# Kernel optimization log

Measured on AMD Instinct MI355X. Metric: run time of the kernel, lower is better.

## Reference

```python
import jax, jax.numpy as jnp
import numpy as np
import math

B, S, D, H = 4, 2048, 1024, 16
HD = D // H  # head_dim = 64


def setup_inputs() -> dict:
    key = jax.random.key(0)
    ks = jax.random.split(key, 12)
    inv = 1.0 / math.sqrt(D)
    inp = {
        "query": jax.random.normal(ks[0], (B, S, D), dtype=jnp.float32),
        "key": jax.random.normal(ks[1], (B, S, D), dtype=jnp.float32),
        "value": jax.random.normal(ks[2], (B, S, D), dtype=jnp.float32),
        # causal mask, broadcast over heads; guarantees no all-masked softmax rows
        "mask": jnp.tril(jnp.ones((S, S), dtype=jnp.int32))[None, None].repeat(B, axis=0),
        # linear params stored as (in, out); y = x @ W + b (same math as torch Linear)
        "Wq": jax.random.uniform(ks[3], (D, D), jnp.float32, -inv, inv),
        "bq": jax.random.uniform(ks[4], (D,), jnp.float32, -inv, inv),
        "Wk": jax.random.uniform(ks[5], (D, D), jnp.float32, -inv, inv),
        "bk": jax.random.uniform(ks[6], (D,), jnp.float32, -inv, inv),
        "Wv": jax.random.uniform(ks[7], (D, D), jnp.float32, -inv, inv),
        "bv": jax.random.uniform(ks[8], (D,), jnp.float32, -inv, inv),
        "Wo": jax.random.uniform(ks[9], (D, D), jnp.float32, -inv, inv),
        "bo": jax.random.uniform(ks[10], (D,), jnp.float32, -inv, inv),
    }
    return inp


def _split_heads(x):
    # [B, S, D] -> [B, H, S, HD]
    b, s, _ = x.shape
    return x.reshape(b, s, H, HD).transpose(0, 2, 1, 3)


def reference(query, key, value, mask, Wq, bq, Wk, bk, Wv, bv, Wo, bo):
    q = _split_heads(query @ Wq + bq)   # [B,H,S,HD]
    k = _split_heads(key @ Wk + bk)
    v = _split_heads(value @ Wv + bv)
    scores = jnp.einsum("bhqd,bhkd->bhqk", q, k)          # [B,H,S,S]
    scores = jnp.where(mask == 0, -jnp.inf, scores)
    attn = jax.nn.softmax(scores / math.sqrt(HD), axis=-1)
    attn = attn * mask.astype(attn.dtype)                  # post-softmax re-mask (as in source)
    out = jnp.einsum("bhqk,bhkd->bhqd", attn, v)           # [B,H,S,HD]
    out = out.transpose(0, 2, 1, 3).reshape(query.shape[0], -1, D)
    return out @ Wo + bo
```

## Files before the change

kernel.cpp:

```cpp
#include <hip/hip_runtime.h>

typedef __attribute__((ext_vector_type(8))) short short8;
typedef __attribute__((ext_vector_type(8))) unsigned short ushort8;
typedef __attribute__((ext_vector_type(4))) unsigned short us4;
typedef __attribute__((ext_vector_type(4))) float f32x4;
typedef __attribute__((ext_vector_type(4))) int i32x4;

#define S_LEN 2048
#define D_MODEL 1024
#define N_HEADS 16
#define HEAD_DIM 64

__device__ __forceinline__ unsigned short f2bf(float f) {
  union { float f; unsigned u; } x; x.f = f;
  unsigned r = x.u + 0x7FFFu + ((x.u >> 16) & 1u);
  return (unsigned short)(r >> 16);
}

__device__ __forceinline__ int pkbf(float a, float b) {
  union { float f; unsigned u; } x, y;
  x.f = a; y.f = b;
  return (int)__builtin_amdgcn_perm(y.u + 0x8000u, x.u + 0x8000u, 0x07060302u);
}

__global__ __launch_bounds__(256) void cvt3_kernel(const float* __restrict__ a,
                                                   const float* __restrict__ b,
                                                   const float* __restrict__ c,
                                                   unsigned short* __restrict__ oa,
                                                   unsigned short* __restrict__ ob,
                                                   unsigned short* __restrict__ oc) {
  int bid = blockIdx.x;
  const float* in = (bid < 4096) ? a : (bid < 8192 ? b : c);
  unsigned short* out = (bid < 4096) ? oa : (bid < 8192 ? ob : oc);
  int i = (bid & 4095) * 256 + threadIdx.x;
  const f32x4* in4 = (const f32x4*)in;
  f32x4 x = in4[2 * i], y = in4[2 * i + 1];
  i32x4 o;
  o[0] = pkbf(x[0], x[1]);
  o[1] = pkbf(x[2], x[3]);
  o[2] = pkbf(y[0], y[1]);
  o[3] = pkbf(y[2], y[3]);
  ((i32x4*)out)[i] = o;
}

__global__ __launch_bounds__(256) void transpose_w4(
    const float* __restrict__ Wq, const float* __restrict__ Wk,
    const float* __restrict__ Wv, const float* __restrict__ Wo,
    unsigned short* __restrict__ wqkvT, unsigned short* __restrict__ woT) {
  __shared__ float tile[64][65];
  const int z = blockIdx.z;
  const float* W = (z == 0) ? Wq : (z == 1) ? Wk : (z == 2) ? Wv : Wo;
  unsigned short* Wt = (z < 3) ? (wqkvT + (size_t)z * D_MODEL * D_MODEL) : woT;
  const int no = blockIdx.x * 64, ko = blockIdx.y * 64;
  const int tx = threadIdx.x & 63, ty = threadIdx.x >> 6;
  for (int r = ty; r < 64; r += 4)
    tile[r][tx] = W[(size_t)(ko + r) * D_MODEL + no + tx];
  __syncthreads();
  for (int r = ty; r < 64; r += 4)
    Wt[(size_t)(no + r) * D_MODEL + ko + tx] = f2bf(tile[tx][r]);
}

template <int MODE>
__global__ __launch_bounds__(256, (MODE == 0 ? 2 : 3)) void proj_gemm(
    const unsigned short* __restrict__ A0,
    const unsigned short* __restrict__ A1,
    const unsigned short* __restrict__ A2,
    const unsigned short* __restrict__ Bt,
    const float* __restrict__ b0p, const float* __restrict__ b1p,
    const float* __restrict__ b2p,
    void* __restrict__ o0, void* __restrict__ o1, void* __restrict__ o2,
    float qscale) {
  constexpr int NJ = (MODE == 0) ? 8 : 4;
  constexpr int BN = NJ * 32;
  constexpr int BUFS = 4096 + NJ * 1024;
  constexpr int NBI = NJ / 2;
  extern __shared__ __align__(16) unsigned short smem_d[];
  const int tid = threadIdx.x;
  const int wave = tid >> 6, lane = tid & 63;
  const int quad = lane >> 4, l16 = lane & 15;

  const int GX = (MODE == 0) ? 12 : 8;
  const int nlin = blockIdx.y * GX + blockIdx.x;
  const int xcd = nlin & 7;
  const int j = nlin >> 3;
  int bx_eff, by_eff;
  if (MODE == 0) { by_eff = xcd * 8 + j / 12; bx_eff = j % 12; }
  else           { by_eff = xcd * 8 + (j >> 3); bx_eff = j & 7; }
  const int m0 = by_eff * 128, n0 = bx_eff * BN;
  const int wm = (wave >> 1) * 64, wn = (wave & 1) * (NJ * 16);

  const int sel = (MODE == 0) ? (n0 >> 10) : 0;
  const unsigned short* A = (MODE == 0) ? (sel == 0 ? A0 : sel == 1 ? A1 : A2) : A0;
  const float* bias = (MODE == 0) ? (sel == 0 ? b0p : sel == 1 ? b1p : b2p) : b0p;
  const float scale = (MODE == 0 && sel == 0) ? qscale : 1.0f;
  const int nb = (MODE == 0) ? (n0 & 1023) : n0;

  f32x4 acc[4][NJ] = {};

  const int lrow = lane >> 2;
  const int kcs = ((lane & 3) ^ ((lane >> 3) & 3)) << 3;

  auto stage = [&](int kt, int bsel) {
    unsigned short* Ab = smem_d + bsel * BUFS;
    unsigned short* Bb = Ab + 4096;
    const int k0 = kt * 32;
#pragma unroll
    for (int c = 0; c < 2; ++c) {
      const int r = wave * 32 + c * 16;
      const unsigned short* ga = A + (size_t)(m0 + r + lrow) * D_MODEL + k0 + kcs;
      __builtin_amdgcn_global_load_lds((const __attribute__((address_space(1))) void*)ga,
          (__attribute__((address_space(3))) void*)(Ab + r * 32), 16, 0, 0);
    }
#pragma unroll
    for (int c = 0; c < NBI; ++c) {
      const int r = wave * (BN / 4) + c * 16;
      const unsigned short* gb = Bt + (size_t)(n0 + r + lrow) * D_MODEL + k0 + kcs;
      __builtin_amdgcn_global_load_lds((const __attribute__((address_space(1))) void*)gb,
          (__attribute__((address_space(3))) void*)(Bb + r * 32), 16, 0, 0);
    }
  };

  const int fsw = (quad ^ ((l16 >> 1) & 3)) << 3;

  stage(0, 0); stage(1, 1); stage(2, 2);
  if constexpr (MODE == 0) { asm volatile("s_waitcnt vmcnt(12)" ::: "memory"); }
  else                     { asm volatile("s_waitcnt vmcnt(8)" ::: "memory"); }
  __builtin_amdgcn_s_barrier();
  __builtin_amdgcn_sched_barrier(0);

  for (int kt = 0; kt < 32; ++kt) {
    const int bsel = kt % 3;
    const unsigned short* Ab = smem_d + bsel * BUFS;
    const unsigned short* Bb = Ab + 4096;
    short8 af[4], bf[NJ];
#pragma unroll
    for (int i = 0; i < 4; ++i)
      af[i] = *(const short8*)(Ab + (wm + i * 16 + l16) * 32 + fsw);
#pragma unroll
    for (int j2 = 0; j2 < NJ; ++j2)
      bf[j2] = *(const short8*)(Bb + (wn + j2 * 16 + l16) * 32 + fsw);
    asm volatile("s_waitcnt lgkmcnt(0)" ::: "memory");
    __builtin_amdgcn_s_barrier();
    __builtin_amdgcn_sched_barrier(0);
    if (kt + 3 < 32) stage(kt + 3, bsel);
    __builtin_amdgcn_s_setprio(1);
#pragma unroll
    for (int i = 0; i < 4; ++i)
#pragma unroll
      for (int j2 = 0; j2 < NJ; ++j2)
        acc[i][j2] = __builtin_amdgcn_mfma_f32_16x16x32_bf16(af[i], bf[j2], acc[i][j2], 0, 0, 0);
    __builtin_amdgcn_s_setprio(0);
    if constexpr (MODE == 0) {
      if (kt + 3 < 32)      { asm volatile("s_waitcnt vmcnt(12)" ::: "memory"); }
      else if (kt + 2 < 32) { asm volatile("s_waitcnt vmcnt(6)" ::: "memory"); }
      else if (kt + 1 < 32) { asm volatile("s_waitcnt vmcnt(0)" ::: "memory"); }
    } else {
      if (kt + 3 < 32)      { asm volatile("s_waitcnt vmcnt(8)" ::: "memory"); }
      else if (kt + 2 < 32) { asm volatile("s_waitcnt vmcnt(4)" ::: "memory"); }
      else if (kt + 1 < 32) { asm volatile("s_waitcnt vmcnt(0)" ::: "memory"); }
    }
    __builtin_amdgcn_s_barrier();
    __builtin_amdgcn_sched_barrier(0);
  }

  float bv[NJ];
#pragma unroll
  for (int j2 = 0; j2 < NJ; ++j2) bv[j2] = bias[nb + wn + j2 * 16 + l16];

  if constexpr (MODE == 0) {
    if (sel < 2) {
      unsigned short* T = smem_d + wave * 2176;
      unsigned short* out = (unsigned short*)(sel == 0 ? o0 : o1);
      const int h0 = (nb + wn) >> 6;
#pragma unroll
      for (int i = 0; i < 4; ++i) {
#pragma unroll
        for (int j2 = 0; j2 < 8; ++j2)
#pragma unroll
          for (int r = 0; r < 4; ++r)
            T[(quad * 4 + r) * 136 + j2 * 16 + l16] = f2bf((acc[i][j2][r] + bv[j2]) * scale);
        int m = m0 + wm + i * 16 + l16;
        int b = m >> 11, s = m & 2047;
#pragma unroll
        for (int t = 0; t < 4; ++t) {
          short8 row = *(const short8*)(T + l16 * 136 + t * 32 + quad * 8);
          int c = t * 32 + quad * 8;
          int h = h0 + (c >> 6), d = c & 63;
          *(short8*)(out + (((size_t)(b * N_HEADS + h) * S_LEN + s) << 6) + d) = row;
        }
      }
    } else {
      unsigned short* vt = (unsigned short*)o2;
#pragma unroll
      for (int i = 0; i < 4; ++i) {
        int m = m0 + wm + i * 16 + quad * 4;
        int b = m >> 11, s = m & 2047;
#pragma unroll
        for (int j2 = 0; j2 < 8; ++j2) {
          int n = nb + wn + j2 * 16 + l16;
          int h = n >> 6, d = n & 63;
          us4 pv;
#pragma unroll
          for (int r = 0; r < 4; ++r) pv[r] = f2bf(acc[i][j2][r] + bv[j2]);
          *(us4*)(vt + (((size_t)(b * N_HEADS + h) * 64 + d) << 11) + s) = pv;
        }
      }
    }
  } else {
    float* Tf = (float*)smem_d + wave * 1088;
    float* out = (float*)o0;
#pragma unroll
    for (int i = 0; i < 4; ++i) {
#pragma unroll
      for (int j2 = 0; j2 < 4; ++j2)
#pragma unroll
        for (int r = 0; r < 4; ++r)
          Tf[(quad * 4 + r) * 68 + j2 * 16 + l16] = acc[i][j2][r] + bv[j2];
      int m = m0 + wm + i * 16 + l16;
#pragma unroll
      for (int t = 0; t < 4; ++t) {
        f32x4 row = *(const f32x4*)(Tf + l16 * 68 + t * 16 + quad * 4);
        *(f32x4*)(out + (size_t)m * D_MODEL + nb + wn + t * 16 + quad * 4) = row;
      }
    }
  }
}

__global__ __launch_bounds__(256, 4) void flash_attn(
    const unsigned short* __restrict__ Qh,
    const unsigned short* __restrict__ Kh,
    const unsigned short* __restrict__ Vt,
    unsigned short* __restrict__ ctx) {
  __shared__ __align__(16) unsigned short smem[16384];
  const int tid = threadIdx.x;
  const int wave = tid >> 6, lane = tid & 63;
  const int quad = lane >> 4, l16 = lane & 15;
  const int l7 = l16 & 7;

  const int nlin = blockIdx.y * 16 + blockIdx.x;
  const int xcd = nlin & 7;
  const int rr = nlin >> 3;
  const int bh = xcd * 8 + (rr & 7);
  const int qslot = rr >> 3;
  const int qa = qslot & 3, qb = qslot >> 2;
  const int qbase = qa + ((qb >> 1) << 2);
  const int qi = (qb & 1) ? (15 - qbase) : qbase;
  const int q0 = qi * 128;
  const int nk = 2 * qi + 2;
  const size_t hb = (size_t)bh * (S_LEN * HEAD_DIM);
  const int srow = lane >> 3;
  const int schunk = ((lane & 7) ^ srow) * 8;

  auto stage = [&](int kt, int buf) {
    unsigned short* Kb = smem + buf * 8192;
    unsigned short* Vb = smem + buf * 8192 + 4096;
#pragma unroll
    for (int c = 0; c < 2; ++c) {
      int row = wave * 16 + c * 8 + srow;
      const unsigned short* gk = Kh + hb + (size_t)(kt * 64 + row) * 64 + schunk;
      __builtin_amdgcn_global_load_lds((const __attribute__((address_space(1))) void*)gk,
          (__attribute__((address_space(3))) void*)(Kb + (wave * 16 + c * 8) * 64), 16, 0, 0);
      const unsigned short* gv = Vt + hb + (size_t)row * S_LEN + kt * 64 + schunk;
      __builtin_amdgcn_global_load_lds((const __attribute__((address_space(1))) void*)gv,
          (__attribute__((address_space(3))) void*)(Vb + (wave * 16 + c * 8) * 64), 16, 0, 0);
    }
  };

  stage(0, 0);

  short8 qf[2][2];
#pragma unroll
  for (int s = 0; s < 2; ++s)
#pragma unroll
    for (int t = 0; t < 2; ++t)
      qf[s][t] = *(const short8*)(Qh + hb +
          (size_t)(q0 + wave * 32 + s * 16 + l16) * 64 + t * 32 + quad * 8);

  f32x4 o[4][2] = {};
  float rsum[2] = {0.f, 0.f};

  for (int kt = 0; kt < nk; ++kt) {
    __syncthreads();
    if (kt + 1 < nk) stage(kt + 1, (kt + 1) & 1);
    const unsigned short* Kb = smem + (kt & 1) * 8192;
    const unsigned short* Vb = Kb + 4096;

    if (kt * 64 > q0 + wave * 32 + 31) continue;

    f32x4 sc[2][4];
    __builtin_amdgcn_s_setprio(1);
#pragma unroll
    for (int nt = 0; nt < 4; ++nt) {
      short8 k0 = *(const short8*)(Kb + (nt * 16 + l16) * 64 + ((quad ^ l7) << 3));
      short8 k1 = *(const short8*)(Kb + (nt * 16 + l16) * 64 + (((4 + quad) ^ l7) << 3));
#pragma unroll
      for (int s = 0; s < 2; ++s) {
        f32x4 z = {};
        z = __builtin_amdgcn_mfma_f32_16x16x32_bf16(k0, qf[s][0], z, 0, 0, 0);
        sc[s][nt] = __builtin_amdgcn_mfma_f32_16x16x32_bf16(k1, qf[s][1], z, 0, 0, 0);
      }
    }
    __builtin_amdgcn_s_setprio(0);
    if (kt >= 2 * qi) {
#pragma unroll
      for (int s = 0; s < 2; ++s) {
        int qg = q0 + wave * 32 + s * 16 + l16;
#pragma unroll
        for (int nt = 0; nt < 4; ++nt) {
          int kg = kt * 64 + nt * 16 + quad * 4;
#pragma unroll
          for (int r = 0; r < 4; ++r)
            if (kg + r > qg) sc[s][nt][r] = -1e30f;
        }
      }
    }

    union { int i[4]; short8 v; } pf[2][2];
#pragma unroll
    for (int s = 0; s < 2; ++s) {
      int pk[4][2];
#pragma unroll
      for (int nt = 0; nt < 4; ++nt) {
        float p0 = __builtin_amdgcn_exp2f(sc[s][nt][0]);
        float p1 = __builtin_amdgcn_exp2f(sc[s][nt][1]);
        float p2 = __builtin_amdgcn_exp2f(sc[s][nt][2]);
        float p3 = __builtin_amdgcn_exp2f(sc[s][nt][3]);
        rsum[s] += (p0 + p1) + (p2 + p3);
        pk[nt][0] = pkbf(p0, p1);
        pk[nt][1] = pkbf(p2, p3);
      }
#pragma unroll
      for (int t = 0; t < 2; ++t) {
        int A = pk[t * 2][0], C = pk[t * 2 + 1][0];
        int B2 = pk[t * 2][1], D = pk[t * 2 + 1][1];
        asm("v_permlane32_swap_b32 %0, %1" : "+v"(A), "+v"(C));
        asm("v_permlane16_swap_b32 %0, %1" : "+v"(A), "+v"(C));
        asm("v_permlane32_swap_b32 %0, %1" : "+v"(B2), "+v"(D));
        asm("v_permlane16_swap_b32 %0, %1" : "+v"(B2), "+v"(D));
        pf[s][t].i[0] = A;
        pf[s][t].i[1] = B2;
        pf[s][t].i[2] = C;
        pf[s][t].i[3] = D;
      }
    }

    __builtin_amdgcn_s_setprio(1);
#pragma unroll
    for (int ntd = 0; ntd < 4; ++ntd) {
      short8 v0 = *(const short8*)(Vb + (ntd * 16 + l16) * 64 + ((quad ^ l7) << 3));
      short8 v1 = *(const short8*)(Vb + (ntd * 16 + l16) * 64 + (((4 + quad) ^ l7) << 3));
#pragma unroll
      for (int s = 0; s < 2; ++s) {
        o[ntd][s] = __builtin_amdgcn_mfma_f32_16x16x32_bf16(v0, pf[s][0].v, o[ntd][s], 0, 0, 0);
        o[ntd][s] = __builtin_amdgcn_mfma_f32_16x16x32_bf16(v1, pf[s][1].v, o[ntd][s], 0, 0, 0);
      }
    }
    __builtin_amdgcn_s_setprio(0);
  }

#pragma unroll
  for (int s = 0; s < 2; ++s) {
    rsum[s] += __shfl_xor(rsum[s], 16, 64);
    rsum[s] += __shfl_xor(rsum[s], 32, 64);
  }

  __syncthreads();
  unsigned short* Os = smem;
#pragma unroll
  for (int s = 0; s < 2; ++s) {
    float invl = 1.0f / rsum[s];
#pragma unroll
    for (int ntd = 0; ntd < 4; ++ntd) {
      us4 pk4;
#pragma unroll
      for (int r = 0; r < 4; ++r) pk4[r] = f2bf(o[ntd][s][r] * invl);
      *(us4*)(Os + (wave * 32 + s * 16 + l16) * 72 + ntd * 16 + quad * 4) = pk4;
    }
  }
  __syncthreads();
  const int b = bh >> 4, h = bh & 15;
#pragma unroll
  for (int it = 0; it < 4; ++it) {
    int e = it * 256 + tid;
    int row = e >> 3, c = (e & 7) * 8;
    short8 vrow = *(const short8*)(Os + row * 72 + c);
    *(short8*)(ctx + (size_t)(b * S_LEN + q0 + row) * D_MODEL + h * HEAD_DIM + c) = vrow;
  }
}

extern "C" void kernel_launch(void* const* d_in, const int* in_sizes, int n_in,
                              void* d_out, int out_size, void* d_ws, size_t ws_size,
                              hipStream_t stream) {
  (void)in_sizes; (void)n_in; (void)out_size;
  const float* q  = (const float*)d_in[0];
  const float* k  = (const float*)d_in[1];
  const float* v  = (const float*)d_in[2];
  const float* Wq = (const float*)d_in[4];
  const float* bq = (const float*)d_in[5];
  const float* Wk = (const float*)d_in[6];
  const float* bk = (const float*)d_in[7];
  const float* Wv = (const float*)d_in[8];
  const float* bv = (const float*)d_in[9];
  const float* Wo = (const float*)d_in[10];
  const float* bo = (const float*)d_in[11];
  float* out = (float*)d_out;

  if (ws_size < 109051904u) return;
  char* ws = (char*)d_ws;
  unsigned short* xq    = (unsigned short*)(ws);
  unsigned short* xk    = (unsigned short*)(ws + 16777216);
  unsigned short* xv    = (unsigned short*)(ws + 33554432);
  unsigned short* wqkvT = (unsigned short*)(ws + 50331648);
  unsigned short* woT   = (unsigned short*)(ws + 56623104);
  unsigned short* qh    = (unsigned short*)(ws + 58720256);
  unsigned short* kh    = qh + 8388608;
  unsigned short* vt    = kh + 8388608;
  unsigned short* ctx   = xq;

  static int attr_done = 0;
  if (!attr_done) {
    auto* k0f = proj_gemm<0>;
    auto* k1f = proj_gemm<1>;
    hipFuncSetAttribute(reinterpret_cast<const void*>(k0f),
                        hipFuncAttributeMaxDynamicSharedMemorySize, 73728);
    hipFuncSetAttribute(reinterpret_cast<const void*>(k1f),
                        hipFuncAttributeMaxDynamicSharedMemorySize, 49152);
    attr_done = 1;
  }

  cvt3_kernel<<<12288, 256, 0, stream>>>(q, k, v, xq, xk, xv);
  transpose_w4<<<dim3(16, 16, 4), 256, 0, stream>>>(Wq, Wk, Wv, Wo, wqkvT, woT);
  proj_gemm<0><<<dim3(12, 64), 256, 73728, stream>>>(xq, xk, xv, wqkvT, bq, bk, bv,
                                                     qh, kh, vt, 0.125f * 1.44269504088896f);
  flash_attn<<<dim3(16, 64), 256, 0, stream>>>(qh, kh, vt, ctx);
  proj_gemm<1><<<dim3(8, 64), 256, 49152, stream>>>(ctx, ctx, ctx, woT, bo, bo, bo,
                                                    out, out, out, 1.0f);
}
```

Measured before the change: 339.7 us.

## Pair causal query tiles per attention block and merge prep kernels

```diff
diff --git a/kernel.cpp b/kernel.cpp
--- a/kernel.cpp
+++ b/kernel.cpp
@@ -23,41 +23,48 @@
   return (int)__builtin_amdgcn_perm(y.u + 0x8000u, x.u + 0x8000u, 0x07060302u);
 }
 
-__global__ __launch_bounds__(256) void cvt3_kernel(const float* __restrict__ a,
-                                                   const float* __restrict__ b,
-                                                   const float* __restrict__ c,
-                                                   unsigned short* __restrict__ oa,
-                                                   unsigned short* __restrict__ ob,
-                                                   unsigned short* __restrict__ oc) {
-  int bid = blockIdx.x;
-  const float* in = (bid < 4096) ? a : (bid < 8192 ? b : c);
-  unsigned short* out = (bid < 4096) ? oa : (bid < 8192 ? ob : oc);
-  int i = (bid & 4095) * 256 + threadIdx.x;
-  const f32x4* in4 = (const f32x4*)in;
-  f32x4 x = in4[2 * i], y = in4[2 * i + 1];
-  i32x4 o;
-  o[0] = pkbf(x[0], x[1]);
-  o[1] = pkbf(x[2], x[3]);
-  o[2] = pkbf(y[0], y[1]);
-  o[3] = pkbf(y[2], y[3]);
-  ((i32x4*)out)[i] = o;
-}
-
-__global__ __launch_bounds__(256) void transpose_w4(
+__device__ __forceinline__ int cvtpk(float a, float b) {
+  int r;
+  asm("v_cvt_pk_bf16_f32 %0, %1, %2" : "=v"(r) : "v"(a), "v"(b));
+  return r;
+}
+
+__global__ __launch_bounds__(256) void prep_kernel(
+    const float* __restrict__ q, const float* __restrict__ k,
+    const float* __restrict__ v,
+    unsigned short* __restrict__ oq, unsigned short* __restrict__ ok,
+    unsigned short* __restrict__ ov,
     const float* __restrict__ Wq, const float* __restrict__ Wk,
     const float* __restrict__ Wv, const float* __restrict__ Wo,
     unsigned short* __restrict__ wqkvT, unsigned short* __restrict__ woT) {
   __shared__ float tile[64][65];
-  const int z = blockIdx.z;
-  const float* W = (z == 0) ? Wq : (z == 1) ? Wk : (z == 2) ? Wv : Wo;
-  unsigned short* Wt = (z < 3) ? (wqkvT + (size_t)z * D_MODEL * D_MODEL) : woT;
-  const int no = blockIdx.x * 64, ko = blockIdx.y * 64;
-  const int tx = threadIdx.x & 63, ty = threadIdx.x >> 6;
-  for (int r = ty; r < 64; r += 4)
-    tile[r][tx] = W[(size_t)(ko + r) * D_MODEL + no + tx];
-  __syncthreads();
-  for (int r = ty; r < 64; r += 4)
-    Wt[(size_t)(no + r) * D_MODEL + ko + tx] = f2bf(tile[tx][r]);
+  const int bid = blockIdx.x;
+  if (bid < 12288) {
+    const float* in = (bid < 4096) ? q : (bid < 8192 ? k : v);
+    unsigned short* out = (bid < 4096) ? oq : (bid < 8192 ? ok : ov);
+    int i = (bid & 4095) * 256 + threadIdx.x;
+    const f32x4* in4 = (const f32x4*)in;
+    f32x4 x = in4[2 * i], y = in4[2 * i + 1];
+    i32x4 o;
+    o[0] = pkbf(x[0], x[1]);
+    o[1] = pkbf(x[2], x[3]);
+    o[2] = pkbf(y[0], y[1]);
+    o[3] = pkbf(y[2], y[3]);
+    ((i32x4*)out)[i] = o;
+  } else {
+    const int t = bid - 12288;
+    const int z = t >> 8;
+    const int tt = t & 255;
+    const float* W = (z == 0) ? Wq : (z == 1) ? Wk : (z == 2) ? Wv : Wo;
+    unsigned short* Wt = (z < 3) ? (wqkvT + (size_t)z * D_MODEL * D_MODEL) : woT;
+    const int no = (tt & 15) * 64, ko = (tt >> 4) * 64;
+    const int tx = threadIdx.x & 63, ty = threadIdx.x >> 6;
+    for (int r = ty; r < 64; r += 4)
+      tile[r][tx] = W[(size_t)(ko + r) * D_MODEL + no + tx];
+    __syncthreads();
+    for (int r = ty; r < 64; r += 4)
+      Wt[(size_t)(no + r) * D_MODEL + ko + tx] = f2bf(tile[tx][r]);
+  }
 }
 
 template <int MODE>
@@ -226,7 +233,7 @@
   }
 }
 
-__global__ __launch_bounds__(256, 4) void flash_attn(
+__global__ __launch_bounds__(256, 2) void flash_attn(
     const unsigned short* __restrict__ Qh,
     const unsigned short* __restrict__ Kh,
     const unsigned short* __restrict__ Vt,
@@ -237,16 +244,16 @@
   const int quad = lane >> 4, l16 = lane & 15;
   const int l7 = l16 & 7;
 
-  const int nlin = blockIdx.y * 16 + blockIdx.x;
+  const int nlin = blockIdx.y * 8 + blockIdx.x;
   const int xcd = nlin & 7;
   const int rr = nlin >> 3;
-  const int bh = xcd * 8 + (rr & 7);
-  const int qslot = rr >> 3;
-  const int qa = qslot & 3, qb = qslot >> 2;
-  const int qbase = qa + ((qb >> 1) << 2);
-  const int qi = (qb & 1) ? (15 - qbase) : qbase;
-  const int q0 = qi * 128;
-  const int nk = 2 * qi + 2;
+  const int lo = rr & 31, hi = rr >> 5;
+  const int hg = lo >> 2;
+  const int pp = (lo & 3) + hi * 4;
+  const int p = (pp < 4) ? pp : 11 - pp;
+  const int bh = xcd * 8 + hg;
+  const int q0A = p * 128, q0B = (15 - p) * 128;
+  const int nkA = 2 * p + 2, nkB = 32 - 2 * p;
   const size_t hb = (size_t)bh * (S_LEN * HEAD_DIM);
   const int srow = lane >> 3;
   const int schunk = ((lane & 7) ^ srow) * 8;
@@ -268,71 +275,64 @@
 
   stage(0, 0);
 
-  short8 qf[2][2];
-#pragma unroll
-  for (int s = 0; s < 2; ++s)
+  short8 qf[4][2];
+#pragma unroll
+  for (int s = 0; s < 4; ++s) {
+    const int q0 = (s < 2) ? q0A : q0B;
 #pragma unroll
     for (int t = 0; t < 2; ++t)
       qf[s][t] = *(const short8*)(Qh + hb +
-          (size_t)(q0 + wave * 32 + s * 16 + l16) * 64 + t * 32 + quad * 8);
-
-  f32x4 o[4][2] = {};
-  float rsum[2] = {0.f, 0.f};
-
-  for (int kt = 0; kt < nk; ++kt) {
+          (size_t)(q0 + wave * 32 + (s & 1) * 16 + l16) * 64 + t * 32 + quad * 8);
+  }
+
+  f32x4 o[4][4] = {};
+  float rsum[4] = {0.f, 0.f, 0.f, 0.f};
+
+  for (int kt = 0; kt < nkB; ++kt) {
     __syncthreads();
-    if (kt + 1 < nk) stage(kt + 1, (kt + 1) & 1);
+    if (kt + 1 < nkB) stage(kt + 1, (kt + 1) & 1);
     const unsigned short* Kb = smem + (kt & 1) * 8192;
     const unsigned short* Vb = Kb + 4096;
 
-    if (kt * 64 > q0 + wave * 32 + 31) continue;
-
-    f32x4 sc[2][4];
-    __builtin_amdgcn_s_setprio(1);
+    const bool actA = (kt * 64 <= q0A + wave * 32 + 31);
+
+    int pk[4][4][2];
 #pragma unroll
     for (int nt = 0; nt < 4; ++nt) {
       short8 k0 = *(const short8*)(Kb + (nt * 16 + l16) * 64 + ((quad ^ l7) << 3));
       short8 k1 = *(const short8*)(Kb + (nt * 16 + l16) * 64 + (((4 + quad) ^ l7) << 3));
 #pragma unroll
-      for (int s = 0; s < 2; ++s) {
+      for (int s = 0; s < 4; ++s) {
+        if (s < 2 && !actA) continue;
         f32x4 z = {};
         z = __builtin_amdgcn_mfma_f32_16x16x32_bf16(k0, qf[s][0], z, 0, 0, 0);
-        sc[s][nt] = __builtin_amdgcn_mfma_f32_16x16x32_bf16(k1, qf[s][1], z, 0, 0, 0);
-      }
-    }
-    __builtin_amdgcn_s_setprio(0);
-    if (kt >= 2 * qi) {
-#pragma unroll
-      for (int s = 0; s < 2; ++s) {
-        int qg = q0 + wave * 32 + s * 16 + l16;
-#pragma unroll
-        for (int nt = 0; nt < 4; ++nt) {
-          int kg = kt * 64 + nt * 16 + quad * 4;
+        z = __builtin_amdgcn_mfma_f32_16x16x32_bf16(k1, qf[s][1], z, 0, 0, 0);
+        const int dstart = (s < 2) ? (nkA - 2) : (nkB - 2);
+        if (kt >= dstart) {
+          const int qg = ((s < 2) ? q0A : q0B) + wave * 32 + (s & 1) * 16 + l16;
+          const int kg = kt * 64 + nt * 16 + quad * 4;
 #pragma unroll
           for (int r = 0; r < 4; ++r)
-            if (kg + r > qg) sc[s][nt][r] = -1e30f;
+            if (kg + r > qg) z[r] = -1e30f;
         }
-      }
-    }
-
-    union { int i[4]; short8 v; } pf[2][2];
-#pragma unroll
-    for (int s = 0; s < 2; ++s) {
-      int pk[4][2];
-#pragma unroll
-      for (int nt = 0; nt < 4; ++nt) {
-        float p0 = __builtin_amdgcn_exp2f(sc[s][nt][0]);
-        float p1 = __builtin_amdgcn_exp2f(sc[s][nt][1]);
-        float p2 = __builtin_amdgcn_exp2f(sc[s][nt][2]);
-        float p3 = __builtin_amdgcn_exp2f(sc[s][nt][3]);
+        float p0 = __builtin_amdgcn_exp2f(z[0]);
+        float p1 = __builtin_amdgcn_exp2f(z[1]);
+        float p2 = __builtin_amdgcn_exp2f(z[2]);
+        float p3 = __builtin_amdgcn_exp2f(z[3]);
         rsum[s] += (p0 + p1) + (p2 + p3);
-        pk[nt][0] = pkbf(p0, p1);
-        pk[nt][1] = pkbf(p2, p3);
-      }
+        pk[s][nt][0] = cvtpk(p0, p1);
+        pk[s][nt][1] = cvtpk(p2, p3);
+      }
+    }
+
+    union { int i[4]; short8 v; } pf[4][2];
+#pragma unroll
+    for (int s = 0; s < 4; ++s) {
+      if (s < 2 && !actA) continue;
 #pragma unroll
       for (int t = 0; t < 2; ++t) {
-        int A = pk[t * 2][0], C = pk[t * 2 + 1][0];
-        int B2 = pk[t * 2][1], D = pk[t * 2 + 1][1];
+        int A = pk[s][t * 2][0], C = pk[s][t * 2 + 1][0];
+        int B2 = pk[s][t * 2][1], D = pk[s][t * 2 + 1][1];
         asm("v_permlane32_swap_b32 %0, %1" : "+v"(A), "+v"(C));
         asm("v_permlane16_swap_b32 %0, %1" : "+v"(A), "+v"(C));
         asm("v_permlane32_swap_b32 %0, %1" : "+v"(B2), "+v"(D));
@@ -350,7 +350,8 @@
       short8 v0 = *(const short8*)(Vb + (ntd * 16 + l16) * 64 + ((quad ^ l7) << 3));
       short8 v1 = *(const short8*)(Vb + (ntd * 16 + l16) * 64 + (((4 + quad) ^ l7) << 3));
 #pragma unroll
-      for (int s = 0; s < 2; ++s) {
+      for (int s = 0; s < 4; ++s) {
+        if (s < 2 && !actA) continue;
         o[ntd][s] = __builtin_amdgcn_mfma_f32_16x16x32_bf16(v0, pf[s][0].v, o[ntd][s], 0, 0, 0);
         o[ntd][s] = __builtin_amdgcn_mfma_f32_16x16x32_bf16(v1, pf[s][1].v, o[ntd][s], 0, 0, 0);
       }
@@ -359,32 +360,37 @@
   }
 
 #pragma unroll
-  for (int s = 0; s < 2; ++s) {
+  for (int s = 0; s < 4; ++s) {
     rsum[s] += __shfl_xor(rsum[s], 16, 64);
     rsum[s] += __shfl_xor(rsum[s], 32, 64);
   }
 
-  __syncthreads();
+  const int b = bh >> 4, h = bh & 15;
   unsigned short* Os = smem;
 #pragma unroll
-  for (int s = 0; s < 2; ++s) {
-    float invl = 1.0f / rsum[s];
-#pragma unroll
-    for (int ntd = 0; ntd < 4; ++ntd) {
-      us4 pk4;
-#pragma unroll
-      for (int r = 0; r < 4; ++r) pk4[r] = f2bf(o[ntd][s][r] * invl);
-      *(us4*)(Os + (wave * 32 + s * 16 + l16) * 72 + ntd * 16 + quad * 4) = pk4;
-    }
-  }
-  __syncthreads();
-  const int b = bh >> 4, h = bh & 15;
-#pragma unroll
-  for (int it = 0; it < 4; ++it) {
-    int e = it * 256 + tid;
-    int row = e >> 3, c = (e & 7) * 8;
-    short8 vrow = *(const short8*)(Os + row * 72 + c);
-    *(short8*)(ctx + (size_t)(b * S_LEN + q0 + row) * D_MODEL + h * HEAD_DIM + c) = vrow;
+  for (int qb = 0; qb < 2; ++qb) {
+    __syncthreads();
+#pragma unroll
+    for (int s2 = 0; s2 < 2; ++s2) {
+      const int s = qb * 2 + s2;
+      float invl = 1.0f / rsum[s];
+#pragma unroll
+      for (int ntd = 0; ntd < 4; ++ntd) {
+        us4 pk4;
+#pragma unroll
+        for (int r = 0; r < 4; ++r) pk4[r] = f2bf(o[ntd][s][r] * invl);
+        *(us4*)(Os + (wave * 32 + s2 * 16 + l16) * 72 + ntd * 16 + quad * 4) = pk4;
+      }
+    }
+    __syncthreads();
+    const int q0 = qb ? q0B : q0A;
+#pragma unroll
+    for (int it = 0; it < 4; ++it) {
+      int e = it * 256 + tid;
+      int row = e >> 3, c = (e & 7) * 8;
+      short8 vrow = *(const short8*)(Os + row * 72 + c);
+      *(short8*)(ctx + (size_t)(b * S_LEN + q0 + row) * D_MODEL + h * HEAD_DIM + c) = vrow;
+    }
   }
 }
 
@@ -428,11 +434,11 @@
     attr_done = 1;
   }
 
-  cvt3_kernel<<<12288, 256, 0, stream>>>(q, k, v, xq, xk, xv);
-  transpose_w4<<<dim3(16, 16, 4), 256, 0, stream>>>(Wq, Wk, Wv, Wo, wqkvT, woT);
+  prep_kernel<<<13312, 256, 0, stream>>>(q, k, v, xq, xk, xv,
+                                         Wq, Wk, Wv, Wo, wqkvT, woT);
   proj_gemm<0><<<dim3(12, 64), 256, 73728, stream>>>(xq, xk, xv, wqkvT, bq, bk, bv,
                                                      qh, kh, vt, 0.125f * 1.44269504088896f);
-  flash_attn<<<dim3(16, 64), 256, 0, stream>>>(qh, kh, vt, ctx);
+  flash_attn<<<dim3(8, 64), 256, 0, stream>>>(qh, kh, vt, ctx);
   proj_gemm<1><<<dim3(8, 64), 256, 49152, stream>>>(ctx, ctx, ctx, woT, bo, bo, bo,
                                                     out, out, out, 1.0f);
 }
```

Measured after the change: 323.2 us. 4.8% less time.
